# Optimization experiments

Hardware: AMD Instinct MI355X
Metric: run time of the kernel (lower is better)

Reference implementation:

```python
import jax, jax.numpy as jnp
import numpy as np

THRESH = 0.3
OUT_THRESH = 0.3
LENS = 0.5  # surrogate-gradient window (ActFun in snn-delays repo)


@jax.custom_vjp
def spike(x):
    # Heaviside spike with rectangular surrogate gradient
    return (x > 0.0).astype(x.dtype)

def _spike_fwd(x):
    return spike(x), x

def _spike_bwd(x, g):
    return (g * (jnp.abs(x) < LENS).astype(g.dtype),)

spike.defvjp(_spike_fwd, _spike_bwd)


def setup_inputs() -> dict:
    key = jax.random.key(0)
    ks = jax.random.split(key, 7)
    B, T, I, H, O = 256, 50, 1024, 2048, 20
    # binary input spikes (rate ~0.2), as an SNN would receive
    inp = (jax.random.uniform(ks[0], (B, T, I)) < 0.2).astype(jnp.float32)
    # Linear(in, out, bias=False) -> weight [out, in], Kaiming-uniform-ish init
    w_ih = jax.random.uniform(ks[1], (H, I), minval=-1.0, maxval=1.0) / np.sqrt(I)
    w_hh = jax.random.uniform(ks[2], (H, H), minval=-1.0, maxval=1.0) / np.sqrt(H)
    w_ho = jax.random.uniform(ks[3], (O, H), minval=-1.0, maxval=1.0) / np.sqrt(H)
    tau_m_h = 0.83 + 0.1 * jax.random.normal(ks[4], (H,))
    tau_m_o = 0.83 + 0.1 * jax.random.normal(ks[5], (O,))
    return {"input": inp, "w_ih": w_ih, "w_hh": w_hh, "w_ho": w_ho,
            "tau_m_h": tau_m_h, "tau_m_o": tau_m_o}


def _rsnn_forward(inp, w_ih, w_hh, w_ho, tau_m_h, tau_m_o):
    B, T, I = inp.shape
    H = w_ih.shape[0]
    O = w_ho.shape[0]
    alpha_h = jnp.exp(-1.0 / tau_m_h)  # [H]
    alpha_o = jnp.exp(-1.0 / tau_m_o)  # [O]
    zH = jnp.zeros((B, H), inp.dtype)
    zO = jnp.zeros((B, O), inp.dtype)

    def step(carry, x_t):
        h_mem, h_spk, o_mem, o_spk, o_sum, mot = carry
        # hidden membrane update: input + recurrent + decayed (reset-gated) mem
        h_mem = (x_t @ w_ih.T) + (h_spk @ w_hh.T) + h_mem * alpha_h * (1.0 - h_spk)
        h_spk = spike(h_mem - THRESH)
        # output membrane update
        o_mem = o_mem * alpha_o * (1.0 - o_spk) + h_spk @ w_ho.T
        o_spk = spike(o_mem - OUT_THRESH)
        o_sum = o_sum + o_spk
        mot = mot + jax.nn.softmax(o_mem, axis=1)
        return (h_mem, h_spk, o_mem, o_spk, o_sum, mot), None

    init = (zH, zH, zO, zO, zO, zO)
    (h_mem, h_spk, o_mem, o_spk, o_sum, mot), _ = jax.lax.scan(
        step, init, jnp.swapaxes(inp, 0, 1))  # scan over time [T,B,I]
    return o_sum / T, mot


def reference(input, w_ih, w_hh, w_ho, tau_m_h, tau_m_o):
    return _rsnn_forward(input, w_ih, w_hh, w_ho, tau_m_h, tau_m_o)
```

## Files before the change

kernel.cpp:

```cpp
#include <hip/hip_runtime.h>
#include <stdint.h>
#include <math.h>


#define B_   256
#define T_   50
#define I_   1024
#define H_   2048
#define O_   20
#define XIN_T  262144
#define XS_BUF 524288
#define WNT 294912
#define WPL 98304

typedef __attribute__((ext_vector_type(4))) int intx4;
typedef long long ll_t;

__device__ __forceinline__ int digit_of(float v, int p) {
  int W = (int)rintf(v * 134217728.0f);
  int c0 = ((W + 128) & 255) - 128;
  int W1 = (W - c0) >> 8;
  int c1 = ((W1 + 128) & 255) - 128;
  int W2 = (W1 - c1) >> 8;
  return (p == 0) ? c0 : (p == 1) ? c1 : W2;
}

__global__ void prep_w(const float* __restrict__ w_ih,
                       const float* __restrict__ w_hh,
                       int8_t* __restrict__ Wtl) {
  int blk = blockIdx.x;
  int n = blk / 9, kg = blk % 9;
  int k9 = (kg * 256 + (int)threadIdx.x) * 4;
  int p = k9 / 3072, kk = k9 % 3072;
  const float* src = (kk < 1024) ? (w_ih + n * I_ + kk)
                                 : (w_hh + n * H_ + (kk - 1024));
  float4 v = *(const float4*)src;
  int d0 = digit_of(v.x, p) & 255;
  int d1 = digit_of(v.y, p) & 255;
  int d2 = digit_of(v.z, p) & 255;
  int d3 = digit_of(v.w, p) & 255;
  int packed = d0 | (d1 << 8) | (d2 << 16) | (d3 << 24);
  size_t off = (size_t)(n >> 5) * WNT + (size_t)p * WPL + (kk >> 6) * 2048 +
               (n & 31) * 64 + (kk & 63);
  *(int*)(Wtl + off) = packed;
}

__global__ void init_k(int8_t* __restrict__ Xin, int8_t* __restrict__ Xs,
                       float* __restrict__ Hm, const float* __restrict__ input,
                       const float* __restrict__ tau_h,
                       const float* __restrict__ tau_o,
                       float* __restrict__ AlphaH, float* __restrict__ AlphaO,
                       const float* __restrict__ w_ho, double* __restrict__ WhoD,
                       float* __restrict__ Om, float* __restrict__ Osp,
                       float* __restrict__ Osu, float* __restrict__ Mo) {
  int id = blockIdx.x * 256 + threadIdx.x;
  {
    int b = id >> 8, i4 = (id & 255) * 4;
    for (int t = 0; t < T_; ++t) {
      float4 v = *(const float4*)(input + ((size_t)(b * T_ + t) << 10) + i4);
      uchar4 pk;
      pk.x = v.x > 0.5f ? 1 : 0;
      pk.y = v.y > 0.5f ? 1 : 0;
      pk.z = v.z > 0.5f ? 1 : 0;
      pk.w = v.w > 0.5f ? 1 : 0;
      *(uchar4*)(Xin + (size_t)t * XIN_T + (b >> 6) * 65536 + (i4 >> 6) * 4096 +
                 (b & 63) * 64 + (i4 & 63)) = pk;
    }
  }
  *(double*)(Xs + (size_t)id * 8) = 0.0;
  *(float4*)(Hm + (size_t)id * 8) = make_float4(0.f, 0.f, 0.f, 0.f);
  *(float4*)(Hm + (size_t)id * 8 + 4) = make_float4(0.f, 0.f, 0.f, 0.f);
  if (id < 64 * O_ * 32) {
    int nt = id / 640, rem = id % 640, o = rem / 32, hl = rem & 31;
    WhoD[id] = (double)w_ho[o * H_ + nt * 32 + hl];
  }
  if (id < H_) AlphaH[id] = (float)exp((double)(-1.0f / tau_h[id]));
  if (id < O_) AlphaO[id] = (float)exp((double)(-1.0f / tau_o[id]));
  if (id < B_ * O_) {
    Om[id] = 0.f; Osp[id] = 0.f; Osu[id] = 0.f; Mo[id] = 0.f;
  }
}

__global__ __launch_bounds__(512, 2) void step_k(
    const int8_t* __restrict__ Wtl, const int8_t* __restrict__ Xin,
    int8_t* __restrict__ Xs, float* __restrict__ Hm, double* __restrict__ Po,
    const double* __restrict__ WhoD, const float* __restrict__ AlphaH,
    const float* __restrict__ AlphaO, float* __restrict__ Om,
    float* __restrict__ Osp, float* __restrict__ Osu, float* __restrict__ Mo,
    int t) {
  __shared__ double WhoL[640];
  __shared__ __align__(16) int8_t red[98304];
  __shared__ int8_t spk_lT[2048];

  const int j = blockIdx.x;
  const int nt = (j & 7) * 8 + ((j >> 3) & 7);
  const int mg = j >> 6;
  const int tid = threadIdx.x;
  const int l = tid & 63, k = tid >> 6;
  const int r_ = l & 15, q = l >> 4;
  const int fcg = k >> 2, kq = k & 3;

  for (int i = tid; i < 640; i += 512) WhoL[i] = WhoD[nt * 640 + i];

  const int fr_e = k & 3;
  const int fc_e = k >> 2;
  const int h_e = nt * 32 + fc_e * 16 + r_;

  const int u0 = kq * 12;
  const int8_t* Bw =
      Wtl + (size_t)nt * WNT + fcg * 1024 + r_ * 64 + q * 16;
  const int arow = r_ * 64 + q * 16;

#define REDP(w, idx) (red + (((w) * 12 + (idx)) * 64 + l) * 16)

  const int8_t* Ain = Xin + (size_t)t * XIN_T + mg * 65536 + arow;
  const int8_t* Asp = Xs + (size_t)(t & 1) * XS_BUF + mg * 131072 + arow;
  int8_t* Xw = Xs + (size_t)((t + 1) & 1) * XS_BUF;

  intx4 acc[4][3];
#pragma unroll
  for (int fr = 0; fr < 4; ++fr)
#pragma unroll
    for (int p = 0; p < 3; ++p) acc[fr][p] = (intx4){0, 0, 0, 0};

  intx4 a[2][4], b[2][3];
  {
    const int8_t* ap = (u0 < 16) ? (Ain + u0 * 4096) : (Asp + (u0 - 16) * 4096);
#pragma unroll
    for (int fr = 0; fr < 4; ++fr) a[0][fr] = *(const intx4*)(ap + fr * 1024);
    const int8_t* bp = Bw + (size_t)u0 * 2048;
#pragma unroll
    for (int p = 0; p < 3; ++p) b[0][p] = *(const intx4*)(bp + p * WPL);
  }
#pragma unroll
  for (int i = 0; i < 12; ++i) {
    const int cur = i & 1, nxt = cur ^ 1;
    if (i < 11) {
      const int un = u0 + i + 1;
      const int8_t* ap =
          (un < 16) ? (Ain + un * 4096) : (Asp + (un - 16) * 4096);
#pragma unroll
      for (int fr = 0; fr < 4; ++fr) a[nxt][fr] = *(const intx4*)(ap + fr * 1024);
      const int8_t* bp = Bw + (size_t)un * 2048;
#pragma unroll
      for (int p = 0; p < 3; ++p) b[nxt][p] = *(const intx4*)(bp + p * WPL);
    }
#pragma unroll
    for (int p = 0; p < 3; ++p)
#pragma unroll
      for (int fr = 0; fr < 4; ++fr)
        acc[fr][p] = __builtin_amdgcn_mfma_i32_16x16x64_i8(
            a[cur][fr], b[cur][p], acc[fr][p], 0, 0, 0);
  }

#pragma unroll
  for (int fr = 0; fr < 4; ++fr)
#pragma unroll
    for (int p = 0; p < 3; ++p)
      *(intx4*)REDP(k, fr * 3 + p) = acc[fr][p];
  __syncthreads();
  {
    const int base = fr_e * 3;
    intx4 s0 = (intx4){0, 0, 0, 0}, s1 = s0, s2 = s0;
#pragma unroll
    for (int w = 0; w < 4; ++w) {
      const int wi = fc_e * 4 + w;
      s0 = s0 + *(const intx4*)REDP(wi, base + 0);
      s1 = s1 + *(const intx4*)REDP(wi, base + 1);
      s2 = s2 + *(const intx4*)REDP(wi, base + 2);
    }
    const float alpha = AlphaH[h_e];
    float* hp_ptr = Hm + h_e * 256 + mg * 64 + fr_e * 16 + q * 4;
    float4 hp4 = *(float4*)hp_ptr;
    float* hp = reinterpret_cast<float*>(&hp4);
    unsigned spkpack = 0;
#pragma unroll
    for (int jj = 0; jj < 4; ++jj) {
      ll_t Sv = (ll_t)s0[jj] + ((ll_t)s1[jj] << 8) + ((ll_t)s2[jj] << 16);
      float M = (float)((double)Sv * 7.450580596923828125e-9);
      float hpv = hp[jj];
      float spf = (hpv - 0.3f) > 0.f ? 1.f : 0.f;
      float hmn = M + hpv * alpha * (1.0f - spf);
      hp[jj] = hmn;
      unsigned spk = (hmn - 0.3f) > 0.f ? 1u : 0u;
      const int brl = fr_e * 16 + q * 4 + jj;
      Xw[mg * 131072 + (h_e >> 6) * 4096 + brl * 64 + (h_e & 63)] =
          (int8_t)spk;
      spkpack |= spk << (8 * jj);
    }
    *(float4*)hp_ptr = hp4;
    *(unsigned*)(spk_lT + (fc_e * 16 + r_) * 64 + fr_e * 16 + q * 4) =
        spkpack;
  }
  __syncthreads();

  if (tid < 256) {
    const int bl = tid >> 2, og = (tid & 3) * 5;
    const double* W0 = WhoL + og * 32;
    double a0 = 0, a1 = 0, a2 = 0, a3 = 0, a4 = 0;
#pragma unroll
    for (int hl = 0; hl < 32; ++hl) {
      double m = (double)spk_lT[hl * 64 + bl];
      a0 += m * W0[hl];
      a1 += m * W0[32 + hl];
      a2 += m * W0[64 + hl];
      a3 += m * W0[96 + hl];
      a4 += m * W0[128 + hl];
    }
    double* dst =
        Po + ((size_t)((t & 1) * 256 + mg * 64 + bl) * 64 + nt) * 20 + og;
    dst[0] = a0; dst[1] = a1; dst[2] = a2; dst[3] = a3; dst[4] = a4;
  } else if (k == 7 && t > 0) {
    float m = -3.0e38f;
    if (l < O_) {
      const double* pp = Po + ((size_t)(((t - 1) & 1) * 256 + j) * 64) * 20 + l;
      double s = 0.0;
#pragma unroll
      for (int n2 = 0; n2 < 64; ++n2) s += pp[n2 * 20];
      m = Om[j * O_ + l] * AlphaO[l] * (1.0f - Osp[j * O_ + l]) + (float)s;
    }
    float mx = m;
#pragma unroll
    for (int off = 16; off > 0; off >>= 1)
      mx = fmaxf(mx, __shfl_xor(mx, off, 32));
    float eo = (l < O_) ? expf(m - mx) : 0.f;
    float se = eo;
#pragma unroll
    for (int off = 16; off > 0; off >>= 1) se += __shfl_xor(se, off, 32);
    if (l < O_) {
      float sp = (m - 0.3f) > 0.f ? 1.f : 0.f;
      Om[j * O_ + l] = m;
      Osp[j * O_ + l] = sp;
      Osu[j * O_ + l] += sp;
      Mo[j * O_ + l] += eo / se;
    }
  }
#undef REDP
}

__global__ void final_k(const double* __restrict__ Po,
                        const float* __restrict__ AlphaO,
                        const float* __restrict__ Om,
                        const float* __restrict__ Osp,
                        const float* __restrict__ Osu,
                        const float* __restrict__ Mo, float* __restrict__ out) {
  __shared__ float om_l[O_];
  const int j = blockIdx.x, tid = threadIdx.x;
  if (tid < O_) {
    const double* pp = Po + ((size_t)(256 + j) * 64) * 20 + tid;
    double s = 0.0;
#pragma unroll
    for (int n2 = 0; n2 < 64; ++n2) s += pp[n2 * 20];
    float r = (float)s;
    float m = Om[j * O_ + tid] * AlphaO[tid] * (1.0f - Osp[j * O_ + tid]) + r;
    om_l[tid] = m;
  }
  __syncthreads();
  if (tid < O_) {
    float m = om_l[tid];
    float mx = om_l[0];
#pragma unroll
    for (int o = 1; o < O_; ++o) mx = fmaxf(mx, om_l[o]);
    float se = 0.f;
#pragma unroll
    for (int o = 0; o < O_; ++o) se += expf(om_l[o] - mx);
    float sp = (m - 0.3f) > 0.f ? 1.f : 0.f;
    out[j * O_ + tid] = (Osu[j * O_ + tid] + sp) / 50.0f;
    out[B_ * O_ + j * O_ + tid] = Mo[j * O_ + tid] + expf(m - mx) / se;
  }
}

extern "C" void kernel_launch(void* const* d_in, const int* in_sizes, int n_in,
                              void* d_out, int out_size, void* d_ws, size_t ws_size,
                              hipStream_t stream) {
  const float* input = (const float*)d_in[0];
  const float* w_ih  = (const float*)d_in[1];
  const float* w_hh  = (const float*)d_in[2];
  const float* w_ho  = (const float*)d_in[3];
  const float* tau_h = (const float*)d_in[4];
  const float* tau_o = (const float*)d_in[5];

  char* ws = (char*)d_ws;
  int8_t* Wtl    = (int8_t*)(ws);
  int8_t* Xin    = (int8_t*)(ws + 18874368);
  int8_t* Xs     = (int8_t*)(ws + 31981568);
  double* Po     = (double*)(ws + 33030144);
  float*  Hm     = (float*)(ws + 38273024);
  double* WhoD   = (double*)(ws + 40370176);
  float*  AlphaH = (float*)(ws + 40697856);
  float*  AlphaO = (float*)(ws + 40706048);
  float*  Om     = (float*)(ws + 40706176);
  float*  Osp    = (float*)(ws + 40726656);
  float*  Osu    = (float*)(ws + 40747136);
  float*  Mo     = (float*)(ws + 40767616);
  float*  out    = (float*)d_out;

  prep_w<<<2048 * 9, 256, 0, stream>>>(w_ih, w_hh, Wtl);
  init_k<<<256, 256, 0, stream>>>(Xin, Xs, Hm, input, tau_h, tau_o, AlphaH,
                                  AlphaO, w_ho, WhoD, Om, Osp, Osu, Mo);
  for (int t = 0; t < T_; ++t) {
    step_k<<<256, 512, 0, stream>>>(Wtl, Xin, Xs, Hm, Po, WhoD, AlphaH, AlphaO,
                                    Om, Osp, Osu, Mo, t);
  }
  final_k<<<256, 64, 0, stream>>>(Po, AlphaO, Om, Osp, Osu, Mo, out);
}
```

Measured before the change: 971.8 us.

## Double threads per step block with split-K across 16 waves and two-phase LDS reduction

Each step block now runs 1024 threads instead of 512. The K loop is split into 6 iterations per wave instead of 12, so more waves share the int8 MFMA work for each time step. Partial sums are reduced through shared memory in two phases that reuse the same buffer, one per 16-column half. The hidden membrane state moves to a per-block layout accessed as float2. The output-layer partial sum over Po is also split across 40 lanes and combined with a shuffle. This cuts the serial latency of each per-timestep launch, at the cost of more barriers and reduced occupancy limits.

```diff
diff --git a/kernel.cpp b/kernel.cpp
--- a/kernel.cpp
+++ b/kernel.cpp
@@ -81,7 +81,7 @@
   }
 }
 
-__global__ __launch_bounds__(512, 2) void step_k(
+__global__ __launch_bounds__(1024, 1) void step_k(
     const int8_t* __restrict__ Wtl, const int8_t* __restrict__ Xin,
     int8_t* __restrict__ Xs, float* __restrict__ Hm, double* __restrict__ Po,
     const double* __restrict__ WhoD, const float* __restrict__ AlphaH,
@@ -98,24 +98,16 @@
   const int tid = threadIdx.x;
   const int l = tid & 63, k = tid >> 6;
   const int r_ = l & 15, q = l >> 4;
-  const int fcg = k >> 2, kq = k & 3;
-
-  for (int i = tid; i < 640; i += 512) WhoL[i] = WhoD[nt * 640 + i];
-
-  const int fr_e = k & 3;
-  const int fc_e = k >> 2;
-  const int h_e = nt * 32 + fc_e * 16 + r_;
-
-  const int u0 = kq * 12;
-  const int8_t* Bw =
-      Wtl + (size_t)nt * WNT + fcg * 1024 + r_ * 64 + q * 16;
+  const int fch = k >> 3, kq = k & 7;
+
+  if (tid < 640) WhoL[tid] = WhoD[nt * 640 + tid];
+
   const int arow = r_ * 64 + q * 16;
-
-#define REDP(w, idx) (red + (((w) * 12 + (idx)) * 64 + l) * 16)
-
   const int8_t* Ain = Xin + (size_t)t * XIN_T + mg * 65536 + arow;
   const int8_t* Asp = Xs + (size_t)(t & 1) * XS_BUF + mg * 131072 + arow;
   int8_t* Xw = Xs + (size_t)((t + 1) & 1) * XS_BUF;
+  const int8_t* Bw = Wtl + (size_t)nt * WNT + fch * 1024 + arow;
+  const int u0 = kq * 6;
 
   intx4 acc[4][3];
 #pragma unroll
@@ -133,12 +125,11 @@
     for (int p = 0; p < 3; ++p) b[0][p] = *(const intx4*)(bp + p * WPL);
   }
 #pragma unroll
-  for (int i = 0; i < 12; ++i) {
+  for (int i = 0; i < 6; ++i) {
     const int cur = i & 1, nxt = cur ^ 1;
-    if (i < 11) {
+    if (i < 5) {
       const int un = u0 + i + 1;
-      const int8_t* ap =
-          (un < 16) ? (Ain + un * 4096) : (Asp + (un - 16) * 4096);
+      const int8_t* ap = (un < 16) ? (Ain + un * 4096) : (Asp + (un - 16) * 4096);
 #pragma unroll
       for (int fr = 0; fr < 4; ++fr) a[nxt][fr] = *(const intx4*)(ap + fr * 1024);
       const int8_t* bp = Bw + (size_t)un * 2048;
@@ -153,45 +144,64 @@
             a[cur][fr], b[cur][p], acc[fr][p], 0, 0, 0);
   }
 
-#pragma unroll
-  for (int fr = 0; fr < 4; ++fr)
-#pragma unroll
-    for (int p = 0; p < 3; ++p)
-      *(intx4*)REDP(k, fr * 3 + p) = acc[fr][p];
-  __syncthreads();
-  {
+#define REDP(s, idx) (red + (((s) * 12 + (idx)) * 64 + l) * 16)
+
+  auto merge_epi = [&](int mw, int fcH) {
+    const int fr_e = mw & 3;
+    const int jh = mw >> 2;
     const int base = fr_e * 3;
     intx4 s0 = (intx4){0, 0, 0, 0}, s1 = s0, s2 = s0;
 #pragma unroll
-    for (int w = 0; w < 4; ++w) {
-      const int wi = fc_e * 4 + w;
-      s0 = s0 + *(const intx4*)REDP(wi, base + 0);
-      s1 = s1 + *(const intx4*)REDP(wi, base + 1);
-      s2 = s2 + *(const intx4*)REDP(wi, base + 2);
-    }
+    for (int s = 0; s < 8; ++s) {
+      s0 = s0 + *(const intx4*)REDP(s, base + 0);
+      s1 = s1 + *(const intx4*)REDP(s, base + 1);
+      s2 = s2 + *(const intx4*)REDP(s, base + 2);
+    }
+    const int h_e = nt * 32 + fcH * 16 + r_;
     const float alpha = AlphaH[h_e];
-    float* hp_ptr = Hm + h_e * 256 + mg * 64 + fr_e * 16 + q * 4;
-    float4 hp4 = *(float4*)hp_ptr;
-    float* hp = reinterpret_cast<float*>(&hp4);
-    unsigned spkpack = 0;
-#pragma unroll
-    for (int jj = 0; jj < 4; ++jj) {
+    float* hm_ptr = Hm + (size_t)j * 2048 + fcH * 1024 + mw * 128 + l * 2;
+    float2 hp2 = *(float2*)hm_ptr;
+    float* hp = reinterpret_cast<float*>(&hp2);
+    unsigned spk01 = 0;
+#pragma unroll
+    for (int jj2 = 0; jj2 < 2; ++jj2) {
+      const int jj = jh * 2 + jj2;
       ll_t Sv = (ll_t)s0[jj] + ((ll_t)s1[jj] << 8) + ((ll_t)s2[jj] << 16);
       float M = (float)((double)Sv * 7.450580596923828125e-9);
-      float hpv = hp[jj];
+      float hpv = hp[jj2];
       float spf = (hpv - 0.3f) > 0.f ? 1.f : 0.f;
       float hmn = M + hpv * alpha * (1.0f - spf);
-      hp[jj] = hmn;
+      hp[jj2] = hmn;
       unsigned spk = (hmn - 0.3f) > 0.f ? 1u : 0u;
       const int brl = fr_e * 16 + q * 4 + jj;
       Xw[mg * 131072 + (h_e >> 6) * 4096 + brl * 64 + (h_e & 63)] =
           (int8_t)spk;
-      spkpack |= spk << (8 * jj);
-    }
-    *(float4*)hp_ptr = hp4;
-    *(unsigned*)(spk_lT + (fc_e * 16 + r_) * 64 + fr_e * 16 + q * 4) =
-        spkpack;
-  }
+      spk01 |= spk << (8 * jj2);
+    }
+    *(float2*)hm_ptr = hp2;
+    *(unsigned short*)(spk_lT + (fcH * 16 + r_) * 64 + fr_e * 16 + q * 4 +
+                       jh * 2) = (unsigned short)spk01;
+  };
+
+  if (k < 8) {
+#pragma unroll
+    for (int fr = 0; fr < 4; ++fr)
+#pragma unroll
+      for (int p = 0; p < 3; ++p)
+        *(intx4*)REDP(k, fr * 3 + p) = acc[fr][p];
+  }
+  __syncthreads();
+  if (k >= 8) merge_epi(k - 8, 0);
+  __syncthreads();
+  if (k >= 8) {
+#pragma unroll
+    for (int fr = 0; fr < 4; ++fr)
+#pragma unroll
+      for (int p = 0; p < 3; ++p)
+        *(intx4*)REDP(k - 8, fr * 3 + p) = acc[fr][p];
+  }
+  __syncthreads();
+  if (k < 8) merge_epi(k, 1);
   __syncthreads();
 
   if (tid < 256) {
@@ -210,15 +220,21 @@
     double* dst =
         Po + ((size_t)((t & 1) * 256 + mg * 64 + bl) * 64 + nt) * 20 + og;
     dst[0] = a0; dst[1] = a1; dst[2] = a2; dst[3] = a3; dst[4] = a4;
-  } else if (k == 7 && t > 0) {
+  } else if (k == 15 && t > 0) {
+    const double* pb = Po + ((size_t)(((t - 1) & 1) * 256 + j) * 64) * 20;
+    double s = 0.0;
+    if (l < 40) {
+      const int half = (l >= 20) ? 1 : 0;
+      const int oo = l - half * 20;
+      const double* pp = pb + (size_t)(half * 32) * 20 + oo;
+#pragma unroll
+      for (int n2 = 0; n2 < 32; ++n2) s += pp[n2 * 20];
+    }
+    double s_hi = __shfl(s, l + 20, 64);
     float m = -3.0e38f;
-    if (l < O_) {
-      const double* pp = Po + ((size_t)(((t - 1) & 1) * 256 + j) * 64) * 20 + l;
-      double s = 0.0;
-#pragma unroll
-      for (int n2 = 0; n2 < 64; ++n2) s += pp[n2 * 20];
-      m = Om[j * O_ + l] * AlphaO[l] * (1.0f - Osp[j * O_ + l]) + (float)s;
-    }
+    if (l < O_)
+      m = Om[j * O_ + l] * AlphaO[l] * (1.0f - Osp[j * O_ + l]) +
+          (float)(s + s_hi);
     float mx = m;
 #pragma unroll
     for (int off = 16; off > 0; off >>= 1)
@@ -299,8 +315,8 @@
   init_k<<<256, 256, 0, stream>>>(Xin, Xs, Hm, input, tau_h, tau_o, AlphaH,
                                   AlphaO, w_ho, WhoD, Om, Osp, Osu, Mo);
   for (int t = 0; t < T_; ++t) {
-    step_k<<<256, 512, 0, stream>>>(Wtl, Xin, Xs, Hm, Po, WhoD, AlphaH, AlphaO,
-                                    Om, Osp, Osu, Mo, t);
+    step_k<<<256, 1024, 0, stream>>>(Wtl, Xin, Xs, Hm, Po, WhoD, AlphaH,
+                                     AlphaO, Om, Osp, Osu, Mo, t);
   }
   final_k<<<256, 64, 0, stream>>>(Po, AlphaO, Om, Osp, Osu, Mo, out);
 }
```

After: 1.139 ms. +17.2%, slower.

## Split int8 digit-plane MFMA work across twelve waves and overlap output softmax

Applied to the files above, without the earlier changes.

The step kernel now launches 768 threads per block. Each of the 12 waves handles one weight digit plane and one K-quarter, so it keeps a 4x2 accumulator tile instead of 4x3, which shortens the serial MFMA chain per wave in this latency-bound per-timestep kernel. The hidden-state buffer is re-indexed per block and thread. The previous step's output-layer reduction and softmax move to a spare wave that runs alongside the hidden epilogue, and its 64-term sum is split across two lane halves. The cost is one block per CU with a larger register budget per thread and more waves competing for LDS during the reduction.

```diff
diff --git a/kernel.cpp b/kernel.cpp
--- a/kernel.cpp
+++ b/kernel.cpp
@@ -81,7 +81,7 @@
   }
 }
 
-__global__ __launch_bounds__(512, 2) void step_k(
+__global__ __launch_bounds__(768, 1) void step_k(
     const int8_t* __restrict__ Wtl, const int8_t* __restrict__ Xin,
     int8_t* __restrict__ Xs, float* __restrict__ Hm, double* __restrict__ Po,
     const double* __restrict__ WhoD, const float* __restrict__ AlphaH,
@@ -98,39 +98,31 @@
   const int tid = threadIdx.x;
   const int l = tid & 63, k = tid >> 6;
   const int r_ = l & 15, q = l >> 4;
-  const int fcg = k >> 2, kq = k & 3;
-
-  for (int i = tid; i < 640; i += 512) WhoL[i] = WhoD[nt * 640 + i];
-
-  const int fr_e = k & 3;
-  const int fc_e = k >> 2;
-  const int h_e = nt * 32 + fc_e * 16 + r_;
-
-  const int u0 = kq * 12;
-  const int8_t* Bw =
-      Wtl + (size_t)nt * WNT + fcg * 1024 + r_ * 64 + q * 16;
+  const int pw = k >> 2, kq = k & 3;
+
+  if (tid < 640) WhoL[tid] = WhoD[nt * 640 + tid];
+
   const int arow = r_ * 64 + q * 16;
-
-#define REDP(w, idx) (red + (((w) * 12 + (idx)) * 64 + l) * 16)
-
   const int8_t* Ain = Xin + (size_t)t * XIN_T + mg * 65536 + arow;
   const int8_t* Asp = Xs + (size_t)(t & 1) * XS_BUF + mg * 131072 + arow;
   int8_t* Xw = Xs + (size_t)((t + 1) & 1) * XS_BUF;
-
-  intx4 acc[4][3];
+  const int8_t* Bw = Wtl + (size_t)nt * WNT + (size_t)pw * WPL + arow;
+  const int u0 = kq * 12;
+
+  intx4 acc[4][2];
 #pragma unroll
   for (int fr = 0; fr < 4; ++fr)
 #pragma unroll
-    for (int p = 0; p < 3; ++p) acc[fr][p] = (intx4){0, 0, 0, 0};
-
-  intx4 a[2][4], b[2][3];
+    for (int fc = 0; fc < 2; ++fc) acc[fr][fc] = (intx4){0, 0, 0, 0};
+
+  intx4 a[2][4], b[2][2];
   {
     const int8_t* ap = (u0 < 16) ? (Ain + u0 * 4096) : (Asp + (u0 - 16) * 4096);
 #pragma unroll
     for (int fr = 0; fr < 4; ++fr) a[0][fr] = *(const intx4*)(ap + fr * 1024);
     const int8_t* bp = Bw + (size_t)u0 * 2048;
-#pragma unroll
-    for (int p = 0; p < 3; ++p) b[0][p] = *(const intx4*)(bp + p * WPL);
+    b[0][0] = *(const intx4*)bp;
+    b[0][1] = *(const intx4*)(bp + 1024);
   }
 #pragma unroll
   for (int i = 0; i < 12; ++i) {
@@ -142,36 +134,40 @@
 #pragma unroll
       for (int fr = 0; fr < 4; ++fr) a[nxt][fr] = *(const intx4*)(ap + fr * 1024);
       const int8_t* bp = Bw + (size_t)un * 2048;
-#pragma unroll
-      for (int p = 0; p < 3; ++p) b[nxt][p] = *(const intx4*)(bp + p * WPL);
-    }
-#pragma unroll
-    for (int p = 0; p < 3; ++p)
+      b[nxt][0] = *(const intx4*)bp;
+      b[nxt][1] = *(const intx4*)(bp + 1024);
+    }
+#pragma unroll
+    for (int fc = 0; fc < 2; ++fc)
 #pragma unroll
       for (int fr = 0; fr < 4; ++fr)
-        acc[fr][p] = __builtin_amdgcn_mfma_i32_16x16x64_i8(
-            a[cur][fr], b[cur][p], acc[fr][p], 0, 0, 0);
-  }
+        acc[fr][fc] = __builtin_amdgcn_mfma_i32_16x16x64_i8(
+            a[cur][fr], b[cur][fc], acc[fr][fc], 0, 0, 0);
+  }
+
+#define REDP(s, idx) (red + (((s) * 8 + (idx)) * 64 + l) * 16)
 
 #pragma unroll
   for (int fr = 0; fr < 4; ++fr)
 #pragma unroll
-    for (int p = 0; p < 3; ++p)
-      *(intx4*)REDP(k, fr * 3 + p) = acc[fr][p];
+    for (int fc = 0; fc < 2; ++fc)
+      *(intx4*)REDP(k, fr * 2 + fc) = acc[fr][fc];
   __syncthreads();
-  {
-    const int base = fr_e * 3;
+
+  if (k < 8) {
+    const int fr_e = k >> 1, fc_e = k & 1;
+    const int base = fr_e * 2 + fc_e;
     intx4 s0 = (intx4){0, 0, 0, 0}, s1 = s0, s2 = s0;
 #pragma unroll
     for (int w = 0; w < 4; ++w) {
-      const int wi = fc_e * 4 + w;
-      s0 = s0 + *(const intx4*)REDP(wi, base + 0);
-      s1 = s1 + *(const intx4*)REDP(wi, base + 1);
-      s2 = s2 + *(const intx4*)REDP(wi, base + 2);
-    }
+      s0 = s0 + *(const intx4*)REDP(w, base);
+      s1 = s1 + *(const intx4*)REDP(4 + w, base);
+      s2 = s2 + *(const intx4*)REDP(8 + w, base);
+    }
+    const int h_e = nt * 32 + fc_e * 16 + r_;
     const float alpha = AlphaH[h_e];
-    float* hp_ptr = Hm + h_e * 256 + mg * 64 + fr_e * 16 + q * 4;
-    float4 hp4 = *(float4*)hp_ptr;
+    float* hm_ptr = Hm + (size_t)(j * 512 + tid) * 4;
+    float4 hp4 = *(float4*)hm_ptr;
     float* hp = reinterpret_cast<float*>(&hp4);
     unsigned spkpack = 0;
 #pragma unroll
@@ -188,9 +184,39 @@
           (int8_t)spk;
       spkpack |= spk << (8 * jj);
     }
-    *(float4*)hp_ptr = hp4;
+    *(float4*)hm_ptr = hp4;
     *(unsigned*)(spk_lT + (fc_e * 16 + r_) * 64 + fr_e * 16 + q * 4) =
         spkpack;
+  } else if (k == 11 && t > 0) {
+    const double* pb = Po + ((size_t)(((t - 1) & 1) * 256 + j) * 64) * 20;
+    double s = 0.0;
+    if (l < 40) {
+      const int half = (l >= 20) ? 1 : 0;
+      const int oo = l - half * 20;
+      const double* pp = pb + (size_t)(half * 32) * 20 + oo;
+#pragma unroll
+      for (int n2 = 0; n2 < 32; ++n2) s += pp[n2 * 20];
+    }
+    double s_hi = __shfl(s, l + 20, 64);
+    float m = -3.0e38f;
+    if (l < O_)
+      m = Om[j * O_ + l] * AlphaO[l] * (1.0f - Osp[j * O_ + l]) +
+          (float)(s + s_hi);
+    float mx = m;
+#pragma unroll
+    for (int off = 16; off > 0; off >>= 1)
+      mx = fmaxf(mx, __shfl_xor(mx, off, 32));
+    float eo = (l < O_) ? expf(m - mx) : 0.f;
+    float se = eo;
+#pragma unroll
+    for (int off = 16; off > 0; off >>= 1) se += __shfl_xor(se, off, 32);
+    if (l < O_) {
+      float sp = (m - 0.3f) > 0.f ? 1.f : 0.f;
+      Om[j * O_ + l] = m;
+      Osp[j * O_ + l] = sp;
+      Osu[j * O_ + l] += sp;
+      Mo[j * O_ + l] += eo / se;
+    }
   }
   __syncthreads();
 
@@ -210,30 +236,6 @@
     double* dst =
         Po + ((size_t)((t & 1) * 256 + mg * 64 + bl) * 64 + nt) * 20 + og;
     dst[0] = a0; dst[1] = a1; dst[2] = a2; dst[3] = a3; dst[4] = a4;
-  } else if (k == 7 && t > 0) {
-    float m = -3.0e38f;
-    if (l < O_) {
-      const double* pp = Po + ((size_t)(((t - 1) & 1) * 256 + j) * 64) * 20 + l;
-      double s = 0.0;
-#pragma unroll
-      for (int n2 = 0; n2 < 64; ++n2) s += pp[n2 * 20];
-      m = Om[j * O_ + l] * AlphaO[l] * (1.0f - Osp[j * O_ + l]) + (float)s;
-    }
-    float mx = m;
-#pragma unroll
-    for (int off = 16; off > 0; off >>= 1)
-      mx = fmaxf(mx, __shfl_xor(mx, off, 32));
-    float eo = (l < O_) ? expf(m - mx) : 0.f;
-    float se = eo;
-#pragma unroll
-    for (int off = 16; off > 0; off >>= 1) se += __shfl_xor(se, off, 32);
-    if (l < O_) {
-      float sp = (m - 0.3f) > 0.f ? 1.f : 0.f;
-      Om[j * O_ + l] = m;
-      Osp[j * O_ + l] = sp;
-      Osu[j * O_ + l] += sp;
-      Mo[j * O_ + l] += eo / se;
-    }
   }
 #undef REDP
 }
@@ -299,7 +301,7 @@
   init_k<<<256, 256, 0, stream>>>(Xin, Xs, Hm, input, tau_h, tau_o, AlphaH,
                                   AlphaO, w_ho, WhoD, Om, Osp, Osu, Mo);
   for (int t = 0; t < T_; ++t) {
-    step_k<<<256, 512, 0, stream>>>(Wtl, Xin, Xs, Hm, Po, WhoD, AlphaH, AlphaO,
+    step_k<<<256, 768, 0, stream>>>(Wtl, Xin, Xs, Hm, Po, WhoD, AlphaH, AlphaO,
                                     Om, Osp, Osu, Mo, t);
   }
   final_k<<<256, 64, 0, stream>>>(Po, AlphaO, Om, Osp, Osu, Mo, out);
```

Result: slower. 1.117 ms (+14.9%).
